# Kernel optimization log

Measured on AMD Instinct MI355X. Metric: run time of the kernel, lower is better.

Reference implementation:

```python
import jax, jax.numpy as jnp
import numpy as np

B, N, C, H = 8, 4096, 256, 8
D = C // H
HID = 4 * C
EPS = 1e-5

def _ln(x, w, b):
    mu = jnp.mean(x, axis=-1, keepdims=True)
    var = jnp.var(x, axis=-1, keepdims=True)
    return (x - mu) * jax.lax.rsqrt(var + EPS) * w + b

def setup_inputs() -> dict:
    key = jax.random.key(0)
    ks = jax.random.split(key, 16)
    s = lambda k, shp, scale=0.02: jax.random.normal(k, shp, dtype=jnp.float32) * scale
    return {
        "input_": jax.random.normal(ks[0], (B, N, C), dtype=jnp.float32),
        "prev_state": jax.random.normal(ks[1], (B, N, C), dtype=jnp.float32),
        "pos_embed": jax.random.normal(ks[2], (1, N, C), dtype=jnp.float32),
        "norm1_w": jnp.ones((C,), jnp.float32), "norm1_b": jnp.zeros((C,), jnp.float32),
        "norm2_w": jnp.ones((C,), jnp.float32), "norm2_b": jnp.zeros((C,), jnp.float32),
        "norm3_w": jnp.ones((C,), jnp.float32), "norm3_b": jnp.zeros((C,), jnp.float32),
        "qkv_input_w": s(ks[3], (3 * C, C)),
        "qkv_state_w": s(ks[4], (3 * C, C)),
        "proj_w": s(ks[5], (C, C)), "proj_b": jnp.zeros((C,), jnp.float32),
        "gate_w": s(ks[6], (C, 2 * C)), "gate_b": jnp.zeros((C,), jnp.float32),
        "fc1_w": s(ks[7], (HID, C)), "fc1_b": jnp.zeros((HID,), jnp.float32),
        "fc2_w": s(ks[8], (C, HID)), "fc2_b": jnp.zeros((C,), jnp.float32),
    }

def reference(input_, prev_state, pos_embed,
              norm1_w, norm1_b, norm2_w, norm2_b, norm3_w, norm3_b,
              qkv_input_w, qkv_state_w, proj_w, proj_b,
              gate_w, gate_b, fc1_w, fc1_b, fc2_w, fc2_b):
    input_pos = input_ + pos_embed
    x_ln = _ln(input_pos, norm1_w, norm1_b)
    s_ln = _ln(prev_state, norm2_w, norm2_b)
    # fused QKV from input and state; torch Linear: x @ W.T
    qkv_i = (x_ln @ qkv_input_w.T).reshape(B, N, 3, H, D).transpose(2, 0, 3, 1, 4)
    qkv_s = (s_ln @ qkv_state_w.T).reshape(B, N, 3, H, D).transpose(2, 0, 3, 1, 4)
    q = qkv_i[0] + qkv_s[0]  # [B,H,N,D]
    k = qkv_i[1] + qkv_s[1]
    v = qkv_i[2] + qkv_s[2]
    phi_q = jax.nn.elu(q) + 1.0
    phi_k = jax.nn.elu(k) + 1.0
    # (phi_q @ phi_k^T) @ v reordered associatively to O(N*D^2)
    kv = jnp.einsum('bhnd,bhne->bhde', phi_k, v)        # [B,H,D,D]
    attn = jnp.einsum('bhnd,bhde->bhne', phi_q, kv)     # [B,H,N,D]
    attn = attn.transpose(0, 2, 1, 3).reshape(B, N, C)
    attn = attn @ proj_w.T + proj_b
    output = input_pos + attn
    stacked = jnp.concatenate([input_, prev_state], axis=2)
    update = jax.nn.sigmoid(stacked @ gate_w.T + gate_b)
    new_state = prev_state * (1.0 - update) + attn * update
    h = _ln(output, norm3_w, norm3_b)
    h = jax.nn.gelu(h @ fc1_w.T + fc1_b, approximate=False) @ fc2_w.T + fc2_b
    output = output + h
    return (output, new_state)
```

## Files before the change

kernel.cpp:

```cpp
#include <hip/hip_runtime.h>
#include <cmath>

typedef unsigned short u16;
typedef __attribute__((ext_vector_type(8))) short short8;
typedef __attribute__((ext_vector_type(4))) float f32x4;
typedef __attribute__((ext_vector_type(4))) u16 u16x4;

__device__ __forceinline__ float b2f(u16 u) {
    unsigned x = ((unsigned)u) << 16;
    return __builtin_bit_cast(float, x);
}
__device__ __forceinline__ u16 f2b(float f) {
    unsigned x = __builtin_bit_cast(unsigned, f);
    unsigned r = (x + 0x7fffu + ((x >> 16) & 1u)) >> 16;
    return (u16)r;
}
__device__ __forceinline__ float loadx(const void* p, size_t i, int f32) {
    return f32 ? ((const float*)p)[i] : b2f(((const u16*)p)[i]);
}
__device__ __forceinline__ void gl_lds16(const void* g, void* l) {
    __builtin_amdgcn_global_load_lds(
        (const __attribute__((address_space(1))) void*)g,
        (__attribute__((address_space(3))) void*)l, 16, 0, 0);
}
__device__ __forceinline__ float gelu_f(float x) {
    float y = 0.7978845608028654f * (x + 0.044715f * x * x * x);
    float e = __expf(2.f * y);
    float t = 1.f - 2.f / (e + 1.f);
    return 0.5f * x * (1.f + t);
}

#define BB 8
#define NN 4096
#define CC 256
#define HH 8
#define DD 32
#define HID 1024
#define MTOK (BB*NN)
#define TOKEL ((size_t)MTOK*CC)
#define TOKELC 8388608

#define WS_INPUT_POS 0u
#define WS_PHIQ   16777216u
#define WS_PHIK   33554432u
#define WS_V      50331648u
#define WS_XLN    67108864u
#define WS_SLN    83886080u
#define WS_OUTPRE 100663296u
#define WS_FLAG   117440512u

#define OFF_QKVI  0u
#define OFF_QKVS  196608u
#define OFF_PROJW 393216u
#define OFF_GATEW 458752u
#define OFF_FC1W  589824u
#define OFF_FC2W  851968u
#define OFF_PROJB 1114112u
#define OFF_GATEB 1114368u
#define OFF_FC1B  1114624u
#define OFF_FC2B  1115648u
#define WTOT      1115904u

__device__ __attribute__((aligned(16))) u16 g_wb[WTOT];
__device__ __attribute__((aligned(16))) u16 g_inb[TOKELC];
__device__ __attribute__((aligned(16))) u16 g_prevb[TOKELC];
__device__ __attribute__((aligned(16))) u16 g_ugate[TOKELC];

__global__ __launch_bounds__(64) void detect_kernel(const u16* __restrict__ in0,
                                                    int* __restrict__ flag)
{
    int t = threadIdx.x;
    u16 w = in0[2 * t];
    int e = (w >> 7) & 0xFF;
    int bad = (e < 64 || e > 192) ? 1 : 0;
    unsigned long long m = __ballot(bad);
    if (t == 0) *flag = (__popcll(m) > 8) ? 1 : 0;
}

__global__ __launch_bounds__(256) void wconv_kernel(
    const void* qkvi, const void* qkvs, const void* projw, const void* gatew,
    const void* fc1w, const void* fc2w, const void* projb, const void* gateb,
    const void* fc1b, const void* fc2b, const int* __restrict__ flagp)
{
    const int f32 = *flagp;
    unsigned i = blockIdx.x * 256 + threadIdx.x;
    if (i >= WTOT) return;
    const void* src; unsigned off;
    if      (i < OFF_QKVS)  { src = qkvi;  off = OFF_QKVI; }
    else if (i < OFF_PROJW) { src = qkvs;  off = OFF_QKVS; }
    else if (i < OFF_GATEW) { src = projw; off = OFF_PROJW; }
    else if (i < OFF_FC1W)  { src = gatew; off = OFF_GATEW; }
    else if (i < OFF_FC2W)  { src = fc1w;  off = OFF_FC1W; }
    else if (i < OFF_PROJB) { src = fc2w;  off = OFF_FC2W; }
    else if (i < OFF_GATEB) { src = projb; off = OFF_PROJB; }
    else if (i < OFF_FC1B)  { src = gateb; off = OFF_GATEB; }
    else if (i < OFF_FC2B)  { src = fc1b;  off = OFF_FC1B; }
    else                    { src = fc2b;  off = OFF_FC2B; }
    g_wb[i] = f2b(loadx(src, i - off, f32));
}

__global__ __launch_bounds__(256) void prep_kernel(
    const void* __restrict__ inp, const void* __restrict__ prev,
    const void* __restrict__ pos,
    const void* __restrict__ w1, const void* __restrict__ b1,
    const void* __restrict__ w2, const void* __restrict__ b2,
    u16* __restrict__ input_pos, u16* __restrict__ x_ln, u16* __restrict__ s_ln,
    const int* __restrict__ flagp)
{
    const int f32 = *flagp;
    const int m = blockIdx.x;
    const int c = threadIdx.x;
    const int n = m & (NN - 1);
    const size_t idx = (size_t)m * CC + c;

    __shared__ float red[8];

    float inr = loadx(inp, idx, f32);
    float ip = inr + loadx(pos, (size_t)n * CC + c, f32);
    g_inb[idx] = f2b(inr);
    float s = ip, s2 = ip * ip;
    #pragma unroll
    for (int o = 32; o; o >>= 1) { s += __shfl_down(s, o, 64); s2 += __shfl_down(s2, o, 64); }
    if ((threadIdx.x & 63) == 0) { int w6 = threadIdx.x >> 6; red[w6] = s; red[4 + w6] = s2; }
    __syncthreads();
    float mu  = (red[0] + red[1] + red[2] + red[3]) * (1.f / 256.f);
    float var = (red[4] + red[5] + red[6] + red[7]) * (1.f / 256.f) - mu * mu;
    float rs = rsqrtf(var + 1e-5f);
    input_pos[idx] = f2b(ip);
    x_ln[idx] = f2b((ip - mu) * rs * loadx(w1, c, f32) + loadx(b1, c, f32));
    __syncthreads();

    float pv = loadx(prev, idx, f32);
    g_prevb[idx] = f2b(pv);
    s = pv; s2 = pv * pv;
    #pragma unroll
    for (int o = 32; o; o >>= 1) { s += __shfl_down(s, o, 64); s2 += __shfl_down(s2, o, 64); }
    if ((threadIdx.x & 63) == 0) { int w6 = threadIdx.x >> 6; red[w6] = s; red[4 + w6] = s2; }
    __syncthreads();
    mu  = (red[0] + red[1] + red[2] + red[3]) * (1.f / 256.f);
    var = (red[4] + red[5] + red[6] + red[7]) * (1.f / 256.f) - mu * mu;
    rs = rsqrtf(var + 1e-5f);
    s_ln[idx] = f2b((pv - mu) * rs * loadx(w2, c, f32) + loadx(b2, c, f32));
}

__global__ __launch_bounds__(256) void ln3_kernel(
    const u16* __restrict__ op, const void* __restrict__ w,
    const void* __restrict__ b, u16* __restrict__ out, const int* __restrict__ flagp)
{
    const int f32 = *flagp;
    const size_t m = blockIdx.x;
    const int c = threadIdx.x;
    const size_t idx = m * CC + c;
    __shared__ float red[8];
    float x = b2f(op[idx]);
    float s = x, s2 = x * x;
    #pragma unroll
    for (int o = 32; o; o >>= 1) { s += __shfl_down(s, o, 64); s2 += __shfl_down(s2, o, 64); }
    if ((threadIdx.x & 63) == 0) { int w6 = threadIdx.x >> 6; red[w6] = s; red[4 + w6] = s2; }
    __syncthreads();
    float mu  = (red[0] + red[1] + red[2] + red[3]) * (1.f / 256.f);
    float var = (red[4] + red[5] + red[6] + red[7]) * (1.f / 256.f) - mu * mu;
    out[idx] = f2b((x - mu) * rsqrtf(var + 1e-5f) * loadx(w, c, f32) + loadx(b, c, f32));
}

__global__ __launch_bounds__(64) void kv_mfma(
    const u16* __restrict__ phik_t, const u16* __restrict__ v_t,
    float* __restrict__ kvout)
{
    const int bh = blockIdx.x;
    const int k0 = blockIdx.y * 256;
    const int lane = threadIdx.x;
    const int quad = lane >> 4, lr = lane & 15;

    const u16* A = phik_t + (size_t)bh * DD * NN;
    const u16* W = v_t    + (size_t)bh * DD * NN;

    f32x4 acc[2][2];
    #pragma unroll
    for (int i = 0; i < 2; ++i)
        #pragma unroll
        for (int j = 0; j < 2; ++j) { f32x4 z = {0.f,0.f,0.f,0.f}; acc[i][j] = z; }

    for (int kk = k0; kk < k0 + 256; kk += 32) {
        short8 a0 = *(const short8*)(A + (size_t)lr * NN + kk + quad * 8);
        short8 a1 = *(const short8*)(A + (size_t)(16 + lr) * NN + kk + quad * 8);
        short8 w0 = *(const short8*)(W + (size_t)lr * NN + kk + quad * 8);
        short8 w1 = *(const short8*)(W + (size_t)(16 + lr) * NN + kk + quad * 8);
        acc[0][0] = __builtin_amdgcn_mfma_f32_16x16x32_bf16(a0, w0, acc[0][0], 0, 0, 0);
        acc[0][1] = __builtin_amdgcn_mfma_f32_16x16x32_bf16(a0, w1, acc[0][1], 0, 0, 0);
        acc[1][0] = __builtin_amdgcn_mfma_f32_16x16x32_bf16(a1, w0, acc[1][0], 0, 0, 0);
        acc[1][1] = __builtin_amdgcn_mfma_f32_16x16x32_bf16(a1, w1, acc[1][1], 0, 0, 0);
    }
    float* base = kvout + (size_t)bh * (DD * DD);
    #pragma unroll
    for (int i = 0; i < 2; ++i)
        #pragma unroll
        for (int j = 0; j < 2; ++j)
            #pragma unroll
            for (int r = 0; r < 4; ++r)
                atomicAdd(base + (i * 16 + quad * 4 + r) * DD + j * 16 + lr, acc[i][j][r]);
}

__global__ __launch_bounds__(256) void attn_mfma(
    const u16* __restrict__ phiq, const float* __restrict__ kv,
    u16* __restrict__ attn_tok)
{
    const int bh = blockIdx.x;
    const int b = bh >> 3, h = bh & 7;
    const int wv = threadIdx.x >> 6, lane = threadIdx.x & 63;
    const int quad = lane >> 4, lr = lane & 15;

    const float* kvb = kv + (size_t)bh * (DD * DD);
    short8 bf0, bf1;
    #pragma unroll
    for (int j = 0; j < 8; ++j) {
        int d = quad * 8 + j;
        bf0[j] = (short)f2b(kvb[d * DD + lr]);
        bf1[j] = (short)f2b(kvb[d * DD + 16 + lr]);
    }

    const u16* qb = phiq + (size_t)bh * NN * DD;
    const int n0 = blockIdx.y * 512 + wv * 128;
    #pragma unroll
    for (int t = 0; t < 8; ++t) {
        const int nt = n0 + t * 16;
        short8 af = *(const short8*)(qb + (size_t)(nt + lr) * DD + quad * 8);
        f32x4 c0 = {0.f,0.f,0.f,0.f}, c1 = {0.f,0.f,0.f,0.f};
        c0 = __builtin_amdgcn_mfma_f32_16x16x32_bf16(af, bf0, c0, 0, 0, 0);
        c1 = __builtin_amdgcn_mfma_f32_16x16x32_bf16(af, bf1, c1, 0, 0, 0);
        size_t base = ((size_t)b * NN + nt + quad * 4) * CC + h * DD;
        #pragma unroll
        for (int r = 0; r < 4; ++r) {
            attn_tok[base + (size_t)r * CC + lr]      = f2b(c0[r]);
            attn_tok[base + (size_t)r * CC + 16 + lr] = f2b(c1[r]);
        }
    }
}

#define BM 128
#define BN 128
#define BK 32

template <int MODE>
__global__ __launch_bounds__(256) void gemm_bt(
    const u16* __restrict__ A1in, const u16* __restrict__ A2in,
    int lda, int ldw, int K, int Ksplit, int wcol2,
    u16* __restrict__ o0, u16* __restrict__ o1,
    const u16* __restrict__ xa, const void* __restrict__ xr,
    void* __restrict__ oraw, const int* __restrict__ flagp)
{
    __shared__ __attribute__((aligned(16))) u16 ash[3][BM * BK];
    __shared__ __attribute__((aligned(16))) u16 bsh[3][BN * BK];

    const int f32 = (MODE == 1 || MODE == 4) ? *flagp : 0;

    const u16* W1; const u16* W2; const u16* bias = nullptr;
    if (MODE == 0)      { W1 = g_wb + OFF_QKVI; W2 = g_wb + OFF_QKVS; }
    else if (MODE == 1) { W1 = W2 = g_wb + OFF_PROJW; bias = g_wb + OFF_PROJB; }
    else if (MODE == 3) { W1 = W2 = g_wb + OFF_FC1W;  bias = g_wb + OFF_FC1B; }
    else                { W1 = W2 = g_wb + OFF_FC2W;  bias = g_wb + OFF_FC2B; }

    const int gx = gridDim.x;
    const int nwg = gx * (int)gridDim.y;
    const int hw = blockIdx.y * gx + blockIdx.x;
    const int qq = nwg >> 3, rr = nwg & 7;
    const int xc = hw & 7, pp = hw >> 3;
    const int nid = (xc < rr ? xc * (qq + 1) : rr * (qq + 1) + (xc - rr) * qq) + pp;
    const int bx = nid % gx, by = nid / gx;

    const bool isGate = (MODE == 0) && (bx >= 6);
    const bool swp = (MODE == 0) ? (bx < 2 || isGate) : true;

    const int tid = threadIdx.x;
    const int lane = tid & 63;
    const int wv = tid >> 6;
    const int wm = wv >> 1, wn = wv & 1;
    const int quad = lane >> 4, lr = lane & 15;

    f32x4 acc[4][4];
    #pragma unroll
    for (int i = 0; i < 4; ++i)
        #pragma unroll
        for (int j = 0; j < 4; ++j) { f32x4 z = {0.f,0.f,0.f,0.f}; acc[i][j] = z; }

    const size_t arow0 = (size_t)by * BM;
    const int nbase_blk = isGate ? (bx - 6) * BN : bx * BN;
    const int ldw_eff = isGate ? 2 * CC : ldw;

    const int srow = lane & 31;
    const int sg   = (lane >> 5) << 3;
    const size_t aoff = (arow0 + wv * 32 + srow) * (size_t)lda + sg;
    const size_t woff = ((size_t)nbase_blk + wv * 32 + srow) * (size_t)ldw_eff + sg;

    auto stage = [&](int buf, int k0) {
        const u16* As; const u16* Ws; int ka, kw;
        if (MODE == 0) {
            if (k0 < Ksplit) { As = isGate ? g_inb   : A1in; ka = k0; }
            else             { As = isGate ? g_prevb : A2in; ka = k0 - Ksplit; }
            if (isGate) { Ws = g_wb + OFF_GATEW; kw = k0; }
            else        { Ws = (k0 < Ksplit) ? W1 : W2;
                          kw = (k0 < Ksplit) ? k0 : k0 - Ksplit; }
        } else {
            As = A1in; Ws = W1; ka = k0; kw = k0;
        }
        const u16* ga = As + aoff + ka;
        u16* la = ash[buf] + (wv << 10);
        gl_lds16(ga, la);
        gl_lds16(ga + 16, la + 512);
        const u16* gw = Ws + woff + kw;
        u16* lb = bsh[buf] + (wv << 10);
        gl_lds16(gw, lb);
        gl_lds16(gw + 16, lb + 512);
    };

    auto compute = [&](int buf) {
        short8 af[4], bf[4];
        #pragma unroll
        for (int i = 0; i < 4; ++i) {
            const int ra = wm * 64 + i * 16 + lr;
            af[i] = *(const short8*)(ash[buf] + ((ra >> 5) << 10) + (quad << 8) + ((ra & 31) << 3));
        }
        #pragma unroll
        for (int j = 0; j < 4; ++j) {
            const int rb = wn * 64 + j * 16 + lr;
            bf[j] = *(const short8*)(bsh[buf] + ((rb >> 5) << 10) + (quad << 8) + ((rb & 31) << 3));
        }
        if (swp) {
            #pragma unroll
            for (int i = 0; i < 4; ++i)
                #pragma unroll
                for (int j = 0; j < 4; ++j)
                    acc[i][j] = __builtin_amdgcn_mfma_f32_16x16x32_bf16(bf[j], af[i], acc[i][j], 0, 0, 0);
        } else {
            #pragma unroll
            for (int i = 0; i < 4; ++i)
                #pragma unroll
                for (int j = 0; j < 4; ++j)
                    acc[i][j] = __builtin_amdgcn_mfma_f32_16x16x32_bf16(af[i], bf[j], acc[i][j], 0, 0, 0);
        }
    };

    const int NT = K / BK;
    stage(0, 0);
    stage(1, BK);
    for (int t = 0; t < NT; ++t) {
        if (t + 2 < NT) {
            stage((t + 2) % 3, (t + 2) * BK);
            asm volatile("s_waitcnt vmcnt(8)" ::: "memory");
        } else if (t + 1 < NT) {
            asm volatile("s_waitcnt vmcnt(4)" ::: "memory");
        } else {
            asm volatile("s_waitcnt vmcnt(0)" ::: "memory");
        }
        __builtin_amdgcn_s_barrier();
        asm volatile("" ::: "memory");
        compute(t % 3);
        asm volatile("" ::: "memory");
        __builtin_amdgcn_s_barrier();
    }

    const int mbase = by * BM + wm * 64;
    const int nbase = nbase_blk + wn * 64;
    constexpr int LDOUT = (MODE == 3) ? HID : CC;

    #pragma unroll
    for (int i = 0; i < 4; ++i) {
        #pragma unroll
        for (int j = 0; j < 4; ++j) {
            if (MODE == 0) {
                if (isGate) {
                    const int m = mbase + i * 16 + lr;
                    const int c0 = nbase + j * 16 + quad * 4;
                    u16x4 b4 = *(const u16x4*)(g_wb + OFF_GATEB + c0);
                    u16x4 p;
                    #pragma unroll
                    for (int r = 0; r < 4; ++r) {
                        float u = 1.f / (1.f + __expf(-(acc[i][j][r] + b2f(b4[r]))));
                        p[r] = f2b(u);
                    }
                    *(u16x4*)(g_ugate + (size_t)m * CC + c0) = p;
                } else if (swp) {
                    const int m = mbase + i * 16 + lr;
                    const int b = m >> 12, n = m & (NN - 1);
                    const int c0 = nbase + j * 16 + quad * 4;
                    const int h = c0 >> 5, d0 = c0 & 31;
                    u16x4 p;
                    #pragma unroll
                    for (int r = 0; r < 4; ++r) {
                        float v = acc[i][j][r];
                        p[r] = f2b((v > 0.f) ? (v + 1.f) : __expf(v));
                    }
                    *(u16x4*)(o0 + (((size_t)b * HH + h) * NN + n) * DD + d0) = p;
                } else {
                    const int c = nbase + j * 16 + lr;
                    const int which = c >> 8, rem = c & 255, h = rem >> 5, d = rem & 31;
                    const int m0 = mbase + i * 16 + quad * 4;
                    const int b = m0 >> 12, n0i = m0 & (NN - 1);
                    u16x4 p;
                    #pragma unroll
                    for (int r = 0; r < 4; ++r) {
                        float v = acc[i][j][r];
                        if (which == 1) v = (v > 0.f) ? (v + 1.f) : __expf(v);
                        p[r] = f2b(v);
                    }
                    u16* dst = o0 + (size_t)which * TOKEL;
                    *(u16x4*)(dst + (((size_t)b * HH + h) * DD + d) * NN + n0i) = p;
                }
            } else {
                const int m = mbase + i * 16 + lr;
                const int c0 = nbase + j * 16 + quad * 4;
                const size_t idx0 = (size_t)m * LDOUT + c0;
                float bias4[4];
                {
                    u16x4 t = *(const u16x4*)(bias + c0);
                    #pragma unroll
                    for (int r = 0; r < 4; ++r) bias4[r] = b2f(t[r]);
                }
                if (MODE == 1) {
                    u16x4 xa4 = *(const u16x4*)(xa + idx0);
                    u16x4 ug4 = *(const u16x4*)(g_ugate + idx0);
                    u16x4 po, pr;
                    float vals[4];
                    #pragma unroll
                    for (int r = 0; r < 4; ++r) {
                        float val = acc[i][j][r] + bias4[r];
                        vals[r] = val;
                        po[r] = f2b(val);
                        pr[r] = f2b(b2f(xa4[r]) + val);
                    }
                    *(u16x4*)(o0 + idx0) = po;
                    *(u16x4*)(o1 + idx0) = pr;
                    if (f32) {
                        f32x4 pv = *(const f32x4*)((const float*)xr + idx0);
                        f32x4 o;
                        #pragma unroll
                        for (int r = 0; r < 4; ++r) {
                            float u = b2f(ug4[r]);
                            o[r] = pv[r] * (1.f - u) + vals[r] * u;
                        }
                        *(f32x4*)((float*)oraw + TOKEL + idx0) = o;
                    } else {
                        u16x4 pv = *(const u16x4*)((const u16*)xr + idx0);
                        u16x4 o;
                        #pragma unroll
                        for (int r = 0; r < 4; ++r) {
                            float u = b2f(ug4[r]);
                            o[r] = f2b(b2f(pv[r]) * (1.f - u) + vals[r] * u);
                        }
                        *(u16x4*)((u16*)oraw + TOKEL + idx0) = o;
                    }
                } else if (MODE == 3) {
                    u16x4 p;
                    #pragma unroll
                    for (int r = 0; r < 4; ++r)
                        p[r] = f2b(gelu_f(acc[i][j][r] + bias4[r]));
                    *(u16x4*)(o0 + idx0) = p;
                } else {
                    u16x4 xa4 = *(const u16x4*)(xa + idx0);
                    if (f32) {
                        f32x4 o;
                        #pragma unroll
                        for (int r = 0; r < 4; ++r)
                            o[r] = b2f(xa4[r]) + acc[i][j][r] + bias4[r];
                        *(f32x4*)((float*)oraw + idx0) = o;
                    } else {
                        u16x4 o;
                        #pragma unroll
                        for (int r = 0; r < 4; ++r)
                            o[r] = f2b(b2f(xa4[r]) + acc[i][j][r] + bias4[r]);
                        *(u16x4*)((u16*)oraw + idx0) = o;
                    }
                }
            }
        }
    }
}

extern "C" void kernel_launch(void* const* d_in, const int* in_sizes, int n_in,
                              void* d_out, int out_size, void* d_ws, size_t ws_size,
                              hipStream_t stream)
{
    const void* input_ = d_in[0];
    const void* prev   = d_in[1];
    const void* pos    = d_in[2];
    const void* n1w = d_in[3];  const void* n1b = d_in[4];
    const void* n2w = d_in[5];  const void* n2b = d_in[6];
    const void* n3w = d_in[7];  const void* n3b = d_in[8];
    const void* qkvi = d_in[9]; const void* qkvs = d_in[10];
    const void* projw = d_in[11]; const void* projb = d_in[12];
    const void* gatew = d_in[13]; const void* gateb = d_in[14];
    const void* fc1w = d_in[15]; const void* fc1b = d_in[16];
    const void* fc2w = d_in[17]; const void* fc2b = d_in[18];

    char* ws = (char*)d_ws;
    u16* input_pos = (u16*)(ws + WS_INPUT_POS);
    u16* phiq  = (u16*)(ws + WS_PHIQ);
    u16* phikt = (u16*)(ws + WS_PHIK);
    u16* vt    = (u16*)(ws + WS_V);
    u16* x_ln = (u16*)(ws + WS_XLN);
    u16* s_ln = (u16*)(ws + WS_SLN);
    u16* attn_tok = x_ln;
    u16* attn_proj = phikt;
    float* kvf = (float*)(ws + WS_SLN);
    u16* ln3o = s_ln;
    u16* outpre = (u16*)(ws + WS_OUTPRE);
    u16* h1 = (u16*)(ws + WS_INPUT_POS);
    int* flagp = (int*)(ws + WS_FLAG);

    detect_kernel<<<1, 64, 0, stream>>>((const u16*)input_, flagp);
    wconv_kernel<<<(WTOT + 255) / 256, 256, 0, stream>>>(
        qkvi, qkvs, projw, gatew, fc1w, fc2w, projb, gateb, fc1b, fc2b, flagp);
    prep_kernel<<<MTOK, 256, 0, stream>>>(input_, prev, pos, n1w, n1b, n2w, n2b,
                                          input_pos, x_ln, s_ln, flagp);
    gemm_bt<0><<<dim3(8, MTOK / BM), 256, 0, stream>>>(
        x_ln, s_ln, CC, CC, 2 * CC, CC, 0,
        phiq, nullptr, nullptr, nullptr, nullptr, flagp);
    hipMemsetAsync((void*)kvf, 0, BB * HH * DD * DD * sizeof(float), stream);
    kv_mfma<<<dim3(BB * HH, 16), 64, 0, stream>>>(phikt, vt, kvf);
    attn_mfma<<<dim3(BB * HH, NN / 512), 256, 0, stream>>>(phiq, kvf, attn_tok);
    gemm_bt<1><<<dim3(CC / BN, MTOK / BM), 256, 0, stream>>>(
        attn_tok, attn_tok, CC, CC, CC, CC, 0,
        attn_proj, outpre, input_pos, prev, d_out, flagp);
    ln3_kernel<<<MTOK, 256, 0, stream>>>(outpre, n3w, n3b, ln3o, flagp);
    gemm_bt<3><<<dim3(HID / BN, MTOK / BM), 256, 0, stream>>>(
        ln3o, ln3o, CC, CC, CC, CC, 0,
        h1, nullptr, nullptr, nullptr, nullptr, flagp);
    gemm_bt<4><<<dim3(CC / BN, MTOK / BM), 256, 0, stream>>>(
        h1, h1, HID, HID, HID, HID, 0,
        nullptr, nullptr, outpre, nullptr, d_out, flagp);
}
```

Before: 517.4 us.

## Move gate GEMM into proj GEMM, vectorize layernorm kernels, blend state in LN3

```diff
diff --git a/kernel.cpp b/kernel.cpp
--- a/kernel.cpp
+++ b/kernel.cpp
@@ -108,59 +108,165 @@
     const int* __restrict__ flagp)
 {
     const int f32 = *flagp;
-    const int m = blockIdx.x;
-    const int c = threadIdx.x;
+    const int m = blockIdx.x * 4 + (threadIdx.x >> 6);
+    const int lane = threadIdx.x & 63;
+    const int e0 = lane * 4;
     const int n = m & (NN - 1);
-    const size_t idx = (size_t)m * CC + c;
-
-    __shared__ float red[8];
-
-    float inr = loadx(inp, idx, f32);
-    float ip = inr + loadx(pos, (size_t)n * CC + c, f32);
-    g_inb[idx] = f2b(inr);
-    float s = ip, s2 = ip * ip;
-    #pragma unroll
-    for (int o = 32; o; o >>= 1) { s += __shfl_down(s, o, 64); s2 += __shfl_down(s2, o, 64); }
-    if ((threadIdx.x & 63) == 0) { int w6 = threadIdx.x >> 6; red[w6] = s; red[4 + w6] = s2; }
-    __syncthreads();
-    float mu  = (red[0] + red[1] + red[2] + red[3]) * (1.f / 256.f);
-    float var = (red[4] + red[5] + red[6] + red[7]) * (1.f / 256.f) - mu * mu;
-    float rs = rsqrtf(var + 1e-5f);
-    input_pos[idx] = f2b(ip);
-    x_ln[idx] = f2b((ip - mu) * rs * loadx(w1, c, f32) + loadx(b1, c, f32));
-    __syncthreads();
-
-    float pv = loadx(prev, idx, f32);
-    g_prevb[idx] = f2b(pv);
-    s = pv; s2 = pv * pv;
-    #pragma unroll
-    for (int o = 32; o; o >>= 1) { s += __shfl_down(s, o, 64); s2 += __shfl_down(s2, o, 64); }
-    if ((threadIdx.x & 63) == 0) { int w6 = threadIdx.x >> 6; red[w6] = s; red[4 + w6] = s2; }
-    __syncthreads();
-    mu  = (red[0] + red[1] + red[2] + red[3]) * (1.f / 256.f);
-    var = (red[4] + red[5] + red[6] + red[7]) * (1.f / 256.f) - mu * mu;
-    rs = rsqrtf(var + 1e-5f);
-    s_ln[idx] = f2b((pv - mu) * rs * loadx(w2, c, f32) + loadx(b2, c, f32));
-}
-
-__global__ __launch_bounds__(256) void ln3_kernel(
+    const size_t idx = (size_t)m * CC + e0;
+
+    float inr[4], ip[4];
+    if (f32) {
+        f32x4 a = *(const f32x4*)((const float*)inp + idx);
+        f32x4 p = *(const f32x4*)((const float*)pos + (size_t)n * CC + e0);
+        #pragma unroll
+        for (int r = 0; r < 4; ++r) { inr[r] = a[r]; ip[r] = a[r] + p[r]; }
+    } else {
+        u16x4 a = *(const u16x4*)((const u16*)inp + idx);
+        u16x4 p = *(const u16x4*)((const u16*)pos + (size_t)n * CC + e0);
+        #pragma unroll
+        for (int r = 0; r < 4; ++r) { inr[r] = b2f(a[r]); ip[r] = inr[r] + b2f(p[r]); }
+    }
+    {
+        u16x4 gi;
+        #pragma unroll
+        for (int r = 0; r < 4; ++r) gi[r] = f2b(inr[r]);
+        *(u16x4*)(g_inb + idx) = gi;
+    }
+    float s = 0.f, s2 = 0.f;
+    #pragma unroll
+    for (int r = 0; r < 4; ++r) { s += ip[r]; s2 += ip[r] * ip[r]; }
+    #pragma unroll
+    for (int o = 1; o < 64; o <<= 1) { s += __shfl_xor(s, o, 64); s2 += __shfl_xor(s2, o, 64); }
+    float mu = s * (1.f / 256.f);
+    float rs = rsqrtf(s2 * (1.f / 256.f) - mu * mu + 1e-5f);
+    float wv[4], bv[4];
+    if (f32) {
+        f32x4 w4 = *(const f32x4*)((const float*)w1 + e0);
+        f32x4 b4 = *(const f32x4*)((const float*)b1 + e0);
+        #pragma unroll
+        for (int r = 0; r < 4; ++r) { wv[r] = w4[r]; bv[r] = b4[r]; }
+    } else {
+        u16x4 w4 = *(const u16x4*)((const u16*)w1 + e0);
+        u16x4 b4 = *(const u16x4*)((const u16*)b1 + e0);
+        #pragma unroll
+        for (int r = 0; r < 4; ++r) { wv[r] = b2f(w4[r]); bv[r] = b2f(b4[r]); }
+    }
+    {
+        u16x4 ipo, xo;
+        #pragma unroll
+        for (int r = 0; r < 4; ++r) {
+            ipo[r] = f2b(ip[r]);
+            xo[r]  = f2b((ip[r] - mu) * rs * wv[r] + bv[r]);
+        }
+        *(u16x4*)(input_pos + idx) = ipo;
+        *(u16x4*)(x_ln + idx) = xo;
+    }
+
+    float pv[4];
+    if (f32) {
+        f32x4 a = *(const f32x4*)((const float*)prev + idx);
+        #pragma unroll
+        for (int r = 0; r < 4; ++r) pv[r] = a[r];
+    } else {
+        u16x4 a = *(const u16x4*)((const u16*)prev + idx);
+        #pragma unroll
+        for (int r = 0; r < 4; ++r) pv[r] = b2f(a[r]);
+    }
+    {
+        u16x4 gp;
+        #pragma unroll
+        for (int r = 0; r < 4; ++r) gp[r] = f2b(pv[r]);
+        *(u16x4*)(g_prevb + idx) = gp;
+    }
+    s = 0.f; s2 = 0.f;
+    #pragma unroll
+    for (int r = 0; r < 4; ++r) { s += pv[r]; s2 += pv[r] * pv[r]; }
+    #pragma unroll
+    for (int o = 1; o < 64; o <<= 1) { s += __shfl_xor(s, o, 64); s2 += __shfl_xor(s2, o, 64); }
+    mu = s * (1.f / 256.f);
+    rs = rsqrtf(s2 * (1.f / 256.f) - mu * mu + 1e-5f);
+    if (f32) {
+        f32x4 w4 = *(const f32x4*)((const float*)w2 + e0);
+        f32x4 b4 = *(const f32x4*)((const float*)b2 + e0);
+        #pragma unroll
+        for (int r = 0; r < 4; ++r) { wv[r] = w4[r]; bv[r] = b4[r]; }
+    } else {
+        u16x4 w4 = *(const u16x4*)((const u16*)w2 + e0);
+        u16x4 b4 = *(const u16x4*)((const u16*)b2 + e0);
+        #pragma unroll
+        for (int r = 0; r < 4; ++r) { wv[r] = b2f(w4[r]); bv[r] = b2f(b4[r]); }
+    }
+    {
+        u16x4 so;
+        #pragma unroll
+        for (int r = 0; r < 4; ++r) so[r] = f2b((pv[r] - mu) * rs * wv[r] + bv[r]);
+        *(u16x4*)(s_ln + idx) = so;
+    }
+}
+
+__global__ __launch_bounds__(256) void ln3_blend_kernel(
     const u16* __restrict__ op, const void* __restrict__ w,
-    const void* __restrict__ b, u16* __restrict__ out, const int* __restrict__ flagp)
+    const void* __restrict__ b, u16* __restrict__ out,
+    const u16* __restrict__ ap, const void* __restrict__ prevraw,
+    void* __restrict__ dout, const int* __restrict__ flagp)
 {
     const int f32 = *flagp;
-    const size_t m = blockIdx.x;
-    const int c = threadIdx.x;
-    const size_t idx = m * CC + c;
-    __shared__ float red[8];
-    float x = b2f(op[idx]);
-    float s = x, s2 = x * x;
-    #pragma unroll
-    for (int o = 32; o; o >>= 1) { s += __shfl_down(s, o, 64); s2 += __shfl_down(s2, o, 64); }
-    if ((threadIdx.x & 63) == 0) { int w6 = threadIdx.x >> 6; red[w6] = s; red[4 + w6] = s2; }
-    __syncthreads();
-    float mu  = (red[0] + red[1] + red[2] + red[3]) * (1.f / 256.f);
-    float var = (red[4] + red[5] + red[6] + red[7]) * (1.f / 256.f) - mu * mu;
-    out[idx] = f2b((x - mu) * rsqrtf(var + 1e-5f) * loadx(w, c, f32) + loadx(b, c, f32));
+    const int m = blockIdx.x * 4 + (threadIdx.x >> 6);
+    const int lane = threadIdx.x & 63;
+    const int e0 = lane * 4;
+    const size_t idx = (size_t)m * CC + e0;
+
+    u16x4 x4 = *(const u16x4*)(op + idx);
+    float x[4];
+    #pragma unroll
+    for (int r = 0; r < 4; ++r) x[r] = b2f(x4[r]);
+    float s = 0.f, s2 = 0.f;
+    #pragma unroll
+    for (int r = 0; r < 4; ++r) { s += x[r]; s2 += x[r] * x[r]; }
+    #pragma unroll
+    for (int o = 1; o < 64; o <<= 1) { s += __shfl_xor(s, o, 64); s2 += __shfl_xor(s2, o, 64); }
+    float mu = s * (1.f / 256.f);
+    float rs = rsqrtf(s2 * (1.f / 256.f) - mu * mu + 1e-5f);
+    float wv[4], bv[4];
+    if (f32) {
+        f32x4 w4 = *(const f32x4*)((const float*)w + e0);
+        f32x4 b4 = *(const f32x4*)((const float*)b + e0);
+        #pragma unroll
+        for (int r = 0; r < 4; ++r) { wv[r] = w4[r]; bv[r] = b4[r]; }
+    } else {
+        u16x4 w4 = *(const u16x4*)((const u16*)w + e0);
+        u16x4 b4 = *(const u16x4*)((const u16*)b + e0);
+        #pragma unroll
+        for (int r = 0; r < 4; ++r) { wv[r] = b2f(w4[r]); bv[r] = b2f(b4[r]); }
+    }
+    {
+        u16x4 o4;
+        #pragma unroll
+        for (int r = 0; r < 4; ++r) o4[r] = f2b((x[r] - mu) * rs * wv[r] + bv[r]);
+        *(u16x4*)(out + idx) = o4;
+    }
+
+    u16x4 a4 = *(const u16x4*)(ap + idx);
+    u16x4 u4 = *(const u16x4*)(g_ugate + idx);
+    if (f32) {
+        f32x4 pv = *(const f32x4*)((const float*)prevraw + idx);
+        f32x4 o;
+        #pragma unroll
+        for (int r = 0; r < 4; ++r) {
+            float u = b2f(u4[r]);
+            o[r] = pv[r] * (1.f - u) + b2f(a4[r]) * u;
+        }
+        *(f32x4*)((float*)dout + TOKEL + idx) = o;
+    } else {
+        u16x4 pv = *(const u16x4*)((const u16*)prevraw + idx);
+        u16x4 o;
+        #pragma unroll
+        for (int r = 0; r < 4; ++r) {
+            float u = b2f(u4[r]);
+            o[r] = f2b(b2f(pv[r]) * (1.f - u) + b2f(a4[r]) * u);
+        }
+        *(u16x4*)((u16*)dout + TOKEL + idx) = o;
+    }
 }
 
 __global__ __launch_bounds__(64) void kv_mfma(
@@ -252,7 +358,7 @@
     __shared__ __attribute__((aligned(16))) u16 ash[3][BM * BK];
     __shared__ __attribute__((aligned(16))) u16 bsh[3][BN * BK];
 
-    const int f32 = (MODE == 1 || MODE == 4) ? *flagp : 0;
+    const int f32 = (MODE == 4) ? *flagp : 0;
 
     const u16* W1; const u16* W2; const u16* bias = nullptr;
     if (MODE == 0)      { W1 = g_wb + OFF_QKVI; W2 = g_wb + OFF_QKVS; }
@@ -268,8 +374,8 @@
     const int nid = (xc < rr ? xc * (qq + 1) : rr * (qq + 1) + (xc - rr) * qq) + pp;
     const int bx = nid % gx, by = nid / gx;
 
-    const bool isGate = (MODE == 0) && (bx >= 6);
-    const bool swp = (MODE == 0) ? (bx < 2 || isGate) : true;
+    const bool isGate = (MODE == 1) && (bx >= 2);
+    const bool swp = (MODE == 0) ? (bx < 2) : true;
 
     const int tid = threadIdx.x;
     const int lane = tid & 63;
@@ -284,8 +390,9 @@
         for (int j = 0; j < 4; ++j) { f32x4 z = {0.f,0.f,0.f,0.f}; acc[i][j] = z; }
 
     const size_t arow0 = (size_t)by * BM;
-    const int nbase_blk = isGate ? (bx - 6) * BN : bx * BN;
+    const int nbase_blk = isGate ? (bx - 2) * BN : bx * BN;
     const int ldw_eff = isGate ? 2 * CC : ldw;
+    const int Keff = isGate ? 2 * CC : K;
 
     const int srow = lane & 31;
     const int sg   = (lane >> 5) << 3;
@@ -294,12 +401,12 @@
 
     auto stage = [&](int buf, int k0) {
         const u16* As; const u16* Ws; int ka, kw;
-        if (MODE == 0) {
-            if (k0 < Ksplit) { As = isGate ? g_inb   : A1in; ka = k0; }
-            else             { As = isGate ? g_prevb : A2in; ka = k0 - Ksplit; }
-            if (isGate) { Ws = g_wb + OFF_GATEW; kw = k0; }
-            else        { Ws = (k0 < Ksplit) ? W1 : W2;
-                          kw = (k0 < Ksplit) ? k0 : k0 - Ksplit; }
+        if (isGate) {
+            As = (k0 < CC) ? g_inb : g_prevb; ka = k0 & (CC - 1);
+            Ws = g_wb + OFF_GATEW; kw = k0;
+        } else if (MODE == 0) {
+            if (k0 < Ksplit) { As = A1in; Ws = W1; ka = k0;          kw = k0; }
+            else             { As = A2in; Ws = W2; ka = k0 - Ksplit; kw = k0 - Ksplit; }
         } else {
             As = A1in; Ws = W1; ka = k0; kw = k0;
         }
@@ -340,7 +447,7 @@
         }
     };
 
-    const int NT = K / BK;
+    const int NT = Keff / BK;
     stage(0, 0);
     stage(1, BK);
     for (int t = 0; t < NT; ++t) {
@@ -368,18 +475,7 @@
         #pragma unroll
         for (int j = 0; j < 4; ++j) {
             if (MODE == 0) {
-                if (isGate) {
-                    const int m = mbase + i * 16 + lr;
-                    const int c0 = nbase + j * 16 + quad * 4;
-                    u16x4 b4 = *(const u16x4*)(g_wb + OFF_GATEB + c0);
-                    u16x4 p;
-                    #pragma unroll
-                    for (int r = 0; r < 4; ++r) {
-                        float u = 1.f / (1.f + __expf(-(acc[i][j][r] + b2f(b4[r]))));
-                        p[r] = f2b(u);
-                    }
-                    *(u16x4*)(g_ugate + (size_t)m * CC + c0) = p;
-                } else if (swp) {
+                if (swp) {
                     const int m = mbase + i * 16 + lr;
                     const int b = m >> 12, n = m & (NN - 1);
                     const int c0 = nbase + j * 16 + quad * 4;
@@ -406,6 +502,32 @@
                     u16* dst = o0 + (size_t)which * TOKEL;
                     *(u16x4*)(dst + (((size_t)b * HH + h) * DD + d) * NN + n0i) = p;
                 }
+            } else if (MODE == 1) {
+                const int m = mbase + i * 16 + lr;
+                const int c0 = nbase + j * 16 + quad * 4;
+                const size_t idx0 = (size_t)m * CC + c0;
+                if (isGate) {
+                    u16x4 b4 = *(const u16x4*)(g_wb + OFF_GATEB + c0);
+                    u16x4 p;
+                    #pragma unroll
+                    for (int r = 0; r < 4; ++r) {
+                        float u = 1.f / (1.f + __expf(-(acc[i][j][r] + b2f(b4[r]))));
+                        p[r] = f2b(u);
+                    }
+                    *(u16x4*)(g_ugate + idx0) = p;
+                } else {
+                    u16x4 b4 = *(const u16x4*)(bias + c0);
+                    u16x4 xa4 = *(const u16x4*)(xa + idx0);
+                    u16x4 po, pr;
+                    #pragma unroll
+                    for (int r = 0; r < 4; ++r) {
+                        float val = acc[i][j][r] + b2f(b4[r]);
+                        po[r] = f2b(val);
+                        pr[r] = f2b(b2f(xa4[r]) + val);
+                    }
+                    *(u16x4*)(o0 + idx0) = po;
+                    *(u16x4*)(o1 + idx0) = pr;
+                }
             } else {
                 const int m = mbase + i * 16 + lr;
                 const int c0 = nbase + j * 16 + quad * 4;
@@ -416,40 +538,7 @@
                     #pragma unroll
                     for (int r = 0; r < 4; ++r) bias4[r] = b2f(t[r]);
                 }
-                if (MODE == 1) {
-                    u16x4 xa4 = *(const u16x4*)(xa + idx0);
-                    u16x4 ug4 = *(const u16x4*)(g_ugate + idx0);
-                    u16x4 po, pr;
-                    float vals[4];
-                    #pragma unroll
-                    for (int r = 0; r < 4; ++r) {
-                        float val = acc[i][j][r] + bias4[r];
-                        vals[r] = val;
-                        po[r] = f2b(val);
-                        pr[r] = f2b(b2f(xa4[r]) + val);
-                    }
-                    *(u16x4*)(o0 + idx0) = po;
-                    *(u16x4*)(o1 + idx0) = pr;
-                    if (f32) {
-                        f32x4 pv = *(const f32x4*)((const float*)xr + idx0);
-                        f32x4 o;
-                        #pragma unroll
-                        for (int r = 0; r < 4; ++r) {
-                            float u = b2f(ug4[r]);
-                            o[r] = pv[r] * (1.f - u) + vals[r] * u;
-                        }
-                        *(f32x4*)((float*)oraw + TOKEL + idx0) = o;
-                    } else {
-                        u16x4 pv = *(const u16x4*)((const u16*)xr + idx0);
-                        u16x4 o;
-                        #pragma unroll
-                        for (int r = 0; r < 4; ++r) {
-                            float u = b2f(ug4[r]);
-                            o[r] = f2b(b2f(pv[r]) * (1.f - u) + vals[r] * u);
-                        }
-                        *(u16x4*)((u16*)oraw + TOKEL + idx0) = o;
-                    }
-                } else if (MODE == 3) {
+                if (MODE == 3) {
                     u16x4 p;
                     #pragma unroll
                     for (int r = 0; r < 4; ++r)
@@ -510,18 +599,19 @@
     detect_kernel<<<1, 64, 0, stream>>>((const u16*)input_, flagp);
     wconv_kernel<<<(WTOT + 255) / 256, 256, 0, stream>>>(
         qkvi, qkvs, projw, gatew, fc1w, fc2w, projb, gateb, fc1b, fc2b, flagp);
-    prep_kernel<<<MTOK, 256, 0, stream>>>(input_, prev, pos, n1w, n1b, n2w, n2b,
-                                          input_pos, x_ln, s_ln, flagp);
-    gemm_bt<0><<<dim3(8, MTOK / BM), 256, 0, stream>>>(
+    prep_kernel<<<MTOK / 4, 256, 0, stream>>>(input_, prev, pos, n1w, n1b, n2w, n2b,
+                                              input_pos, x_ln, s_ln, flagp);
+    gemm_bt<0><<<dim3(3 * CC / BN, MTOK / BM), 256, 0, stream>>>(
         x_ln, s_ln, CC, CC, 2 * CC, CC, 0,
         phiq, nullptr, nullptr, nullptr, nullptr, flagp);
     hipMemsetAsync((void*)kvf, 0, BB * HH * DD * DD * sizeof(float), stream);
     kv_mfma<<<dim3(BB * HH, 16), 64, 0, stream>>>(phikt, vt, kvf);
     attn_mfma<<<dim3(BB * HH, NN / 512), 256, 0, stream>>>(phiq, kvf, attn_tok);
-    gemm_bt<1><<<dim3(CC / BN, MTOK / BM), 256, 0, stream>>>(
+    gemm_bt<1><<<dim3(4, MTOK / BM), 256, 0, stream>>>(
         attn_tok, attn_tok, CC, CC, CC, CC, 0,
-        attn_proj, outpre, input_pos, prev, d_out, flagp);
-    ln3_kernel<<<MTOK, 256, 0, stream>>>(outpre, n3w, n3b, ln3o, flagp);
+        attn_proj, outpre, input_pos, nullptr, nullptr, flagp);
+    ln3_blend_kernel<<<MTOK / 4, 256, 0, stream>>>(
+        outpre, n3w, n3b, ln3o, attn_proj, prev, d_out, flagp);
     gemm_bt<3><<<dim3(HID / BN, MTOK / BM), 256, 0, stream>>>(
         ln3o, ln3o, CC, CC, CC, CC, 0,
         h1, nullptr, nullptr, nullptr, nullptr, flagp);
```

After: 428.4 us. -17.2%, faster.
